# Performance work log

Measured on AMD Instinct MI355X. Metric: run time of the kernel, lower is better.

## Reference

```python
import jax, jax.numpy as jnp
import numpy as np

N = 50000
E = 800000
IN_DIM = 128
HID = 128
OUT = 4
EPS = 1e-5


def setup_inputs() -> dict:
    key = jax.random.key(0)
    ks = jax.random.split(key, 16)
    glorot = lambda k, i, o: jax.random.uniform(k, (i, o), jnp.float32, -1.0, 1.0) * jnp.sqrt(6.0 / (i + o))
    return {
        "x": jax.random.normal(ks[0], (N, IN_DIM), jnp.float32),
        "edge_index": jax.random.randint(ks[1], (2, E), 0, N, jnp.int64),
        # SAGEConv layer 0: lin_l (aggregated neighbors, with bias), lin_r (self, no bias)
        "W_l0": glorot(ks[2], IN_DIM, HID), "b_l0": jnp.zeros((HID,), jnp.float32),
        "W_r0": glorot(ks[3], IN_DIM, HID),
        # SAGEConv layer 1
        "W_l1": glorot(ks[4], HID, HID), "b_l1": jnp.zeros((HID,), jnp.float32),
        "W_r1": glorot(ks[5], HID, HID),
        # LayerNorms
        "g0": jnp.ones((HID,), jnp.float32), "beta0": jnp.zeros((HID,), jnp.float32),
        "g1": jnp.ones((HID,), jnp.float32), "beta1": jnp.zeros((HID,), jnp.float32),
        # head
        "W_h": glorot(ks[6], HID, OUT), "b_h": jnp.zeros((OUT,), jnp.float32),
    }


def _sage_conv(x, src, dst, deg_inv, W_l, b_l, W_r):
    # mean-aggregate source features at destination nodes, then project
    agg = jax.ops.segment_sum(x[src], dst, num_segments=N) * deg_inv  # [N, d]
    return agg @ W_l + b_l + x @ W_r


def _layer_norm(x, g, b):
    mu = jnp.mean(x, axis=-1, keepdims=True)
    var = jnp.mean(jnp.square(x - mu), axis=-1, keepdims=True)
    return (x - mu) * jax.lax.rsqrt(var + EPS) * g + b


def reference(x, edge_index, W_l0, b_l0, W_r0, W_l1, b_l1, W_r1, g0, beta0, g1, beta1, W_h, b_h):
    src, dst = edge_index[0], edge_index[1]
    deg = jax.ops.segment_sum(jnp.ones((E,), jnp.float32), dst, num_segments=N)
    deg_inv = (1.0 / jnp.maximum(deg, 1.0))[:, None]  # mean over empty neighborhood -> 0

    h = _sage_conv(x, src, dst, deg_inv, W_l0, b_l0, W_r0)
    h = jax.nn.relu(_layer_norm(h, g0, beta0))
    h = _sage_conv(h, src, dst, deg_inv, W_l1, b_l1, W_r1)
    h = jax.nn.relu(_layer_norm(h, g1, beta1))
    return h @ W_h + b_h  # [N, 4]
```

## Files before the change

### kernel.cpp

```cpp
#include <hip/hip_runtime.h>

#define NN 50000
#define EE 800000
#define DIM 128
#define KK 256
#define OUTD 4
#define EPSV 1e-5f
#define OTS 132
#define NB 196
#define SLOT 8192
#define ACHUNK 4096
#define NA 196

using short8v = __attribute__((ext_vector_type(8))) short;
using f32x4v  = __attribute__((ext_vector_type(4))) float;

__device__ __forceinline__ unsigned short f2bf(float f) {
    union { float f; unsigned u; } x; x.f = f;
    unsigned r = x.u + 0x7FFF + ((x.u >> 16) & 1);
    return (unsigned short)(r >> 16);
}
__device__ __forceinline__ float bf2f(unsigned short u) {
    union { unsigned u; float f; } x; x.u = ((unsigned)u) << 16;
    return x.f;
}

#define XB_BLK 6250
#define W_BLK  256
__global__ __launch_bounds__(256) void prepA_kernel(
    const float* __restrict__ x, ushort* __restrict__ xb,
    const float* __restrict__ Wl0, const float* __restrict__ Wr0,
    const float* __restrict__ Wl1, const float* __restrict__ Wr1,
    ushort* __restrict__ Wt0, ushort* __restrict__ Wt1,
    const int* __restrict__ src, const int* __restrict__ dst,
    int* __restrict__ bucketCursor, unsigned* __restrict__ pairs)
{
    int b = blockIdx.x;
    int tid = threadIdx.x;
    if (b < XB_BLK) {
        int i = b * 256 + tid;
        float4 v = ((const float4*)x)[i];
        ushort4 o;
        o.x = f2bf(v.x); o.y = f2bf(v.y); o.z = f2bf(v.z); o.w = f2bf(v.w);
        ((ushort4*)xb)[i] = o;
        return;
    }
    if (b < XB_BLK + W_BLK) {
        int idx = (b - XB_BLK) * 256 + tid;
        int which = idx >> 15;
        int j = (idx >> 8) & 127;
        int k = idx & 255;
        const float* Wl = which ? Wl1 : Wl0;
        const float* Wr = which ? Wr1 : Wr0;
        ushort* Wt = which ? Wt1 : Wt0;
        float v = (k < 128) ? Wl[k * DIM + j] : Wr[(k - 128) * DIM + j];
        Wt[j * KK + k] = f2bf(v);
        return;
    }

    __shared__ int hist[256];
    __shared__ int scanb[256];
    __shared__ int exStart[256];
    __shared__ int cur2[256];
    __shared__ int gBase[256];
    __shared__ unsigned stage[ACHUNK];
    int ab = b - XB_BLK - W_BLK;
    int eBase = ab * ACHUNK;
    int total = min(ACHUNK, EE - eBase);

    hist[tid] = 0;
    __syncthreads();

    #pragma unroll
    for (int i = 0; i < 16; i++) {
        int idx = i * 256 + tid;
        if (idx < total) {
            int d = dst[eBase + idx];
            atomicAdd(&hist[d >> 8], 1);
        }
    }
    __syncthreads();
    int cntv = hist[tid];
    scanb[tid] = cntv;
    __syncthreads();
    #pragma unroll
    for (int off = 1; off < 256; off <<= 1) {
        int add = (tid >= off) ? scanb[tid - off] : 0;
        __syncthreads();
        scanb[tid] += add;
        __syncthreads();
    }
    int ex = scanb[tid] - cntv;
    exStart[tid] = ex;
    cur2[tid] = ex;
    if (tid < NB) gBase[tid] = (cntv > 0) ? atomicAdd(&bucketCursor[tid], cntv) : 0;
    __syncthreads();

    #pragma unroll
    for (int i = 0; i < 16; i++) {
        int idx = i * 256 + tid;
        if (idx < total) {
            int e = eBase + idx;
            int d = dst[e], s = src[e];
            int bb = d >> 8;
            int sp = atomicAdd(&cur2[bb], 1);
            stage[sp] = ((unsigned)d << 16) | (unsigned)s;
        }
    }
    __syncthreads();

    #pragma unroll
    for (int i = 0; i < 16; i++) {
        int idx = i * 256 + tid;
        if (idx < total) {
            unsigned v = stage[idx];
            int bb = v >> 24;
            int pos = gBase[bb] + (idx - exStart[bb]);
            if (pos < SLOT) pairs[(size_t)bb * SLOT + pos] = v;
        }
    }
}

__global__ __launch_bounds__(256) void passB_kernel(
    const int* __restrict__ bucketCursor,
    const unsigned* __restrict__ pairs,
    int* __restrict__ rowptr, ushort* __restrict__ colS)
{
    __shared__ int bscan[256];
    __shared__ int cw[256];
    __shared__ int pre2[256];
    __shared__ unsigned val_lds[SLOT];
    int tid = threadIdx.x;
    int b = blockIdx.x;

    int c = (tid < NB) ? min(bucketCursor[tid], SLOT) : 0;
    bscan[tid] = c;
    __syncthreads();
    #pragma unroll
    for (int off = 1; off < 256; off <<= 1) {
        int add = (tid >= off) ? bscan[tid - off] : 0;
        __syncthreads();
        bscan[tid] += add;
        __syncthreads();
    }
    int myBase = b ? bscan[b - 1] : 0;
    int count  = bscan[b] - myBase;
    __syncthreads();

    cw[tid] = 0;
    __syncthreads();

    const unsigned* pb = pairs + (size_t)b * SLOT;
    for (int p = tid; p < count; p += 256) {
        unsigned v = pb[p];
        val_lds[p] = v;
        atomicAdd(&cw[(v >> 16) & 255], 1);
    }
    __syncthreads();
    int cnode = cw[tid];
    bscan[tid] = cnode;
    __syncthreads();
    #pragma unroll
    for (int off = 1; off < 256; off <<= 1) {
        int add = (tid >= off) ? bscan[tid - off] : 0;
        __syncthreads();
        bscan[tid] += add;
        __syncthreads();
    }
    int preEx = bscan[tid] - cnode;
    pre2[tid] = preEx;
    int nodeBase = b << 8;
    if (nodeBase + tid < NN) rowptr[nodeBase + tid] = myBase + preEx;
    if (b == NB - 1 && tid == 0) rowptr[NN] = myBase + count;
    cw[tid] = 0;
    __syncthreads();

    for (int p = tid; p < count; p += 256) {
        unsigned v = val_lds[p];
        int dl = (v >> 16) & 255;
        int r = atomicAdd(&cw[dl], 1);
        colS[myBase + pre2[dl] + r] = (ushort)(v & 0xFFFF);
    }
}

template <int DO_HEAD>
__global__ __launch_bounds__(256) void sage_fused_kernel(
    const ushort* __restrict__ featG,
    const int* __restrict__ rowptr, const ushort* __restrict__ colS,
    const ushort* __restrict__ WtB,
    const float* __restrict__ bl,
    const float* __restrict__ g, const float* __restrict__ beta,
    const float* __restrict__ Wh, const float* __restrict__ bh,
    void* __restrict__ outp)
{
    __shared__ __align__(16) char smem[32 * OTS * 4];
    __shared__ float mu_s[32], ri_s[32];
    ushort* featB = (ushort*)smem;
    float*  oT    = (float*)smem;
    #define OT(n, k) oT[(n) * OTS + (k)]

    int tid = threadIdx.x;
    int base = blockIdx.x * 32;
    int lane = tid & 63, w = tid >> 6;

    #pragma unroll
    for (int i = 0; i < 2; i++) {
        int idx = tid + i * 256;
        int n = idx >> 4, c = idx & 15;
        int node = base + n;
        short8v xv = {};
        if (node < NN) xv = *(const short8v*)(featG + (size_t)node * DIM + c * 8);
        int kb = (256 + c * 16) ^ ((n & 7) << 4);
        *(short8v*)(featB + n * KK + (kb >> 1)) = xv;
    }

    {
        int lane16 = lane & 15, grp = lane >> 4;
        int rp = 0;
        {
            int ridx = base + w * 8 + lane;
            if (lane < 9) rp = rowptr[min(ridx, NN)];
        }
        for (int i = 0; i < 8; i++) {
            int n = w * 8 + i;
            int beg = __shfl(rp, i, 64);
            int end = __shfl(rp, i + 1, 64);
            int deg = end - beg;
            float a0[8], a1[8];
            #pragma unroll
            for (int c = 0; c < 8; c++) { a0[c] = 0.f; a1[c] = 0.f; }
            int e = beg + grp;
            for (; e + 4 < end; e += 8) {
                int s0 = colS[e], s1 = colS[e + 4];
                short8v v0 = *(const short8v*)(featG + (size_t)s0 * DIM + lane16 * 8);
                short8v v1 = *(const short8v*)(featG + (size_t)s1 * DIM + lane16 * 8);
                #pragma unroll
                for (int c = 0; c < 8; c++) {
                    a0[c] += bf2f((unsigned short)v0[c]);
                    a1[c] += bf2f((unsigned short)v1[c]);
                }
            }
            if (e < end) {
                int s0 = colS[e];
                short8v v0 = *(const short8v*)(featG + (size_t)s0 * DIM + lane16 * 8);
                #pragma unroll
                for (int c = 0; c < 8; c++) a0[c] += bf2f((unsigned short)v0[c]);
            }
            #pragma unroll
            for (int c = 0; c < 8; c++) {
                a0[c] += a1[c];
                a0[c] += __shfl_xor(a0[c], 16, 64);
                a0[c] += __shfl_xor(a0[c], 32, 64);
            }
            if (grp == 0) {
                float di = 1.0f / fmaxf((float)deg, 1.0f);
                short8v o;
                #pragma unroll
                for (int c = 0; c < 8; c++) o[c] = (short)f2bf(a0[c] * di);
                int kb = (lane16 * 16) ^ ((n & 7) << 4);
                *(short8v*)(featB + n * KK + (kb >> 1)) = o;
            }
        }
    }
    __syncthreads();

    int l15 = lane & 15, q = lane >> 4;
    f32x4v acc00 = {}, acc01 = {}, acc10 = {}, acc11 = {};
    const ushort* wbase = WtB + (size_t)(w * 32) * KK;
    int n0 = l15, n1 = 16 + l15;
    int sw = (l15 & 7) << 4;
    #pragma unroll
    for (int ks = 0; ks < 8; ks++) {
        int kbA = ks * 64 + q * 16;
        short8v a0 = *(const short8v*)(featB + n0 * KK + (((kbA) ^ sw) >> 1));
        short8v a1 = *(const short8v*)(featB + n1 * KK + (((kbA) ^ sw) >> 1));
        int koff = ks * 32 + q * 8;
        short8v b0 = *(const short8v*)(wbase + (size_t)l15 * KK + koff);
        short8v b1 = *(const short8v*)(wbase + (size_t)(16 + l15) * KK + koff);
        acc00 = __builtin_amdgcn_mfma_f32_16x16x32_bf16(a0, b0, acc00, 0, 0, 0);
        acc01 = __builtin_amdgcn_mfma_f32_16x16x32_bf16(a0, b1, acc01, 0, 0, 0);
        acc10 = __builtin_amdgcn_mfma_f32_16x16x32_bf16(a1, b0, acc10, 0, 0, 0);
        acc11 = __builtin_amdgcn_mfma_f32_16x16x32_bf16(a1, b1, acc11, 0, 0, 0);
    }
    __syncthreads();

    {
        int c0 = w * 32 + l15, c1 = c0 + 16;
        float bl0v = bl[c0], bl1v = bl[c1];
        #pragma unroll
        for (int r = 0; r < 4; r++) {
            int r0 = q * 4 + r, r1 = 16 + q * 4 + r;
            OT(r0, c0) = acc00[r] + bl0v;
            OT(r0, c1) = acc01[r] + bl1v;
            OT(r1, c0) = acc10[r] + bl0v;
            OT(r1, c1) = acc11[r] + bl1v;
        }
    }
    __syncthreads();

    {
        int n = tid >> 3, l = tid & 7;
        float s = 0.f, s2 = 0.f;
        #pragma unroll
        for (int kk = 0; kk < 16; kk++) {
            float v = OT(n, l * 16 + kk);
            s += v; s2 += v * v;
        }
        #pragma unroll
        for (int off = 4; off; off >>= 1) {
            s  += __shfl_down(s, off, 8);
            s2 += __shfl_down(s2, off, 8);
        }
        if (l == 0) {
            float mu = s * (1.0f / DIM);
            float var = s2 * (1.0f / DIM) - mu * mu;
            mu_s[n] = mu;
            ri_s[n] = rsqrtf(fmaxf(var, 0.f) + EPSV);
        }
    }
    __syncthreads();

    if (!DO_HEAD) {
        ushort* hout = (ushort*)outp;
        #pragma unroll
        for (int i = 0; i < 16; i++) {
            int idx = tid + i * 256;
            int n = idx >> 7, k = idx & 127;
            int node = base + n;
            if (node < NN) {
                float v = (OT(n, k) - mu_s[n]) * ri_s[n] * g[k] + beta[k];
                hout[(size_t)node * DIM + k] = f2bf(fmaxf(v, 0.f));
            }
        }
    } else {
        float* fout = (float*)outp;
        float vals[16];
        #pragma unroll
        for (int i = 0; i < 16; i++) {
            int idx = tid + i * 256;
            int n = idx >> 7, k = idx & 127;
            float v = (OT(n, k) - mu_s[n]) * ri_s[n] * g[k] + beta[k];
            vals[i] = fmaxf(v, 0.f);
        }
        __syncthreads();
        #pragma unroll
        for (int i = 0; i < 16; i++) {
            int idx = tid + i * 256;
            int n = idx >> 7, k = idx & 127;
            OT(n, k) = vals[i];
        }
        __syncthreads();
        if (tid < 128) {
            int n = tid >> 2, o = tid & 3;
            int node = base + n;
            if (node < NN) {
                float s = bh[o];
                for (int k = 0; k < DIM; k++) s += OT(n, k) * Wh[k * OUTD + o];
                fout[(size_t)node * OUTD + o] = s;
            }
        }
    }
    #undef OT
}

extern "C" void kernel_launch(void* const* d_in, const int* in_sizes, int n_in,
                              void* d_out, int out_size, void* d_ws, size_t ws_size,
                              hipStream_t stream)
{
    const float* x    = (const float*)d_in[0];
    const int*   ei   = (const int*)d_in[1];
    const float* Wl0  = (const float*)d_in[2];
    const float* bl0  = (const float*)d_in[3];
    const float* Wr0  = (const float*)d_in[4];
    const float* Wl1  = (const float*)d_in[5];
    const float* bl1  = (const float*)d_in[6];
    const float* Wr1  = (const float*)d_in[7];
    const float* g0   = (const float*)d_in[8];
    const float* be0  = (const float*)d_in[9];
    const float* g1   = (const float*)d_in[10];
    const float* be1  = (const float*)d_in[11];
    const float* Wh   = (const float*)d_in[12];
    const float* bh   = (const float*)d_in[13];
    float* out = (float*)d_out;

    const int* srcI = ei;
    const int* dstI = ei + EE;

    char* p = (char*)d_ws;
    ushort*   xb     = (ushort*)p;    p += (size_t)NN * DIM * 2;
    ushort*   h      = (ushort*)p;    p += (size_t)NN * DIM * 2;
    ushort*   Wt0    = (ushort*)p;    p += DIM * KK * 2;
    ushort*   Wt1    = (ushort*)p;    p += DIM * KK * 2;
    int*      rowptr = (int*)p;       p += 50016 * 4;
    int*      bucketCursor = (int*)p; p += 256 * 4;
    unsigned* pairs  = (unsigned*)p;  p += (size_t)NB * SLOT * 4;
    ushort*   colS   = (ushort*)p;    p += (size_t)EE * 2;

    hipMemsetAsync(bucketCursor, 0, 256 * sizeof(int), stream);
    prepA_kernel<<<XB_BLK + W_BLK + NA, 256, 0, stream>>>(
        x, xb, Wl0, Wr0, Wl1, Wr1, Wt0, Wt1, srcI, dstI, bucketCursor, pairs);
    passB_kernel<<<NB, 256, 0, stream>>>(bucketCursor, pairs, rowptr, colS);

    const int blocks = (NN + 31) / 32;
    sage_fused_kernel<0><<<blocks, 256, 0, stream>>>(
        xb, rowptr, colS, Wt0, bl0, g0, be0, nullptr, nullptr, (void*)h);
    sage_fused_kernel<1><<<blocks, 256, 0, stream>>>(
        h, rowptr, colS, Wt1, bl1, g1, be1, Wh, bh, (void*)out);
}
```

Before: 214.8 us.

## Split bf16 features into column-quarter planes and gather per-thread by node

```diff
diff --git a/kernel.cpp b/kernel.cpp
--- a/kernel.cpp
+++ b/kernel.cpp
@@ -25,10 +25,11 @@
     return x.f;
 }
 
+
 #define XB_BLK 6250
 #define W_BLK  256
 __global__ __launch_bounds__(256) void prepA_kernel(
-    const float* __restrict__ x, ushort* __restrict__ xb,
+    const float* __restrict__ x, ushort* __restrict__ xqb,
     const float* __restrict__ Wl0, const float* __restrict__ Wr0,
     const float* __restrict__ Wl1, const float* __restrict__ Wr1,
     ushort* __restrict__ Wt0, ushort* __restrict__ Wt1,
@@ -42,7 +43,10 @@
         float4 v = ((const float4*)x)[i];
         ushort4 o;
         o.x = f2bf(v.x); o.y = f2bf(v.y); o.z = f2bf(v.z); o.w = f2bf(v.w);
-        ((ushort4*)xb)[i] = o;
+        int node = i >> 5;
+        int k = (i * 4) & 127;
+        int p = k >> 5, off = k & 31;
+        *(ushort4*)(xqb + ((size_t)p * NN + node) * 32 + off) = o;
         return;
     }
     if (b < XB_BLK + W_BLK) {
@@ -209,57 +213,53 @@
         int n = idx >> 4, c = idx & 15;
         int node = base + n;
         short8v xv = {};
-        if (node < NN) xv = *(const short8v*)(featG + (size_t)node * DIM + c * 8);
+        if (node < NN) {
+            int p = c >> 2;
+            int off = (c & 3) * 8;
+            xv = *(const short8v*)(featG + ((size_t)p * NN + node) * 32 + off);
+        }
         int kb = (256 + c * 16) ^ ((n & 7) << 4);
         *(short8v*)(featB + n * KK + (kb >> 1)) = xv;
     }
 
     {
-        int lane16 = lane & 15, grp = lane >> 4;
-        int rp = 0;
-        {
-            int ridx = base + w * 8 + lane;
-            if (lane < 9) rp = rowptr[min(ridx, NN)];
-        }
-        for (int i = 0; i < 8; i++) {
-            int n = w * 8 + i;
-            int beg = __shfl(rp, i, 64);
-            int end = __shfl(rp, i + 1, 64);
-            int deg = end - beg;
-            float a0[8], a1[8];
+        int n = tid >> 3;
+        int sub = tid & 7;
+        int node = base + n;
+        int beg = 0, end = 0;
+        if (node < NN) { beg = rowptr[node]; end = rowptr[node + 1]; }
+        float di = 1.0f / fmaxf((float)(end - beg), 1.0f);
+        #pragma unroll 1
+        for (int p = 0; p < 4; p++) {
+            const ushort* xq = featG + (size_t)p * NN * 32 + sub * 4;
+            float a0[4], a1[4], a2[4], a3[4];
             #pragma unroll
-            for (int c = 0; c < 8; c++) { a0[c] = 0.f; a1[c] = 0.f; }
-            int e = beg + grp;
-            for (; e + 4 < end; e += 8) {
-                int s0 = colS[e], s1 = colS[e + 4];
-                short8v v0 = *(const short8v*)(featG + (size_t)s0 * DIM + lane16 * 8);
-                short8v v1 = *(const short8v*)(featG + (size_t)s1 * DIM + lane16 * 8);
-                #pragma unroll
-                for (int c = 0; c < 8; c++) {
-                    a0[c] += bf2f((unsigned short)v0[c]);
-                    a1[c] += bf2f((unsigned short)v1[c]);
-                }
+            for (int j = 0; j < 4; j++) { a0[j] = 0.f; a1[j] = 0.f; a2[j] = 0.f; a3[j] = 0.f; }
+            int e = beg;
+            for (; e + 3 < end; e += 4) {
+                int s0 = colS[e], s1 = colS[e + 1], s2 = colS[e + 2], s3 = colS[e + 3];
+                ushort4 v0 = *(const ushort4*)(xq + s0 * 32);
+                ushort4 v1 = *(const ushort4*)(xq + s1 * 32);
+                ushort4 v2 = *(const ushort4*)(xq + s2 * 32);
+                ushort4 v3 = *(const ushort4*)(xq + s3 * 32);
+                a0[0] += bf2f(v0.x); a0[1] += bf2f(v0.y); a0[2] += bf2f(v0.z); a0[3] += bf2f(v0.w);
+                a1[0] += bf2f(v1.x); a1[1] += bf2f(v1.y); a1[2] += bf2f(v1.z); a1[3] += bf2f(v1.w);
+                a2[0] += bf2f(v2.x); a2[1] += bf2f(v2.y); a2[2] += bf2f(v2.z); a2[3] += bf2f(v2.w);
+                a3[0] += bf2f(v3.x); a3[1] += bf2f(v3.y); a3[2] += bf2f(v3.z); a3[3] += bf2f(v3.w);
             }
-            if (e < end) {
+            for (; e < end; e++) {
                 int s0 = colS[e];
-                short8v v0 = *(const short8v*)(featG + (size_t)s0 * DIM + lane16 * 8);
-                #pragma unroll
-                for (int c = 0; c < 8; c++) a0[c] += bf2f((unsigned short)v0[c]);
+                ushort4 v0 = *(const ushort4*)(xq + s0 * 32);
+                a0[0] += bf2f(v0.x); a0[1] += bf2f(v0.y); a0[2] += bf2f(v0.z); a0[3] += bf2f(v0.w);
             }
-            #pragma unroll
-            for (int c = 0; c < 8; c++) {
-                a0[c] += a1[c];
-                a0[c] += __shfl_xor(a0[c], 16, 64);
-                a0[c] += __shfl_xor(a0[c], 32, 64);
-            }
-            if (grp == 0) {
-                float di = 1.0f / fmaxf((float)deg, 1.0f);
-                short8v o;
-                #pragma unroll
-                for (int c = 0; c < 8; c++) o[c] = (short)f2bf(a0[c] * di);
-                int kb = (lane16 * 16) ^ ((n & 7) << 4);
-                *(short8v*)(featB + n * KK + (kb >> 1)) = o;
-            }
+            ushort4 o;
+            float r0 = (a0[0] + a1[0] + a2[0] + a3[0]) * di;
+            float r1 = (a0[1] + a1[1] + a2[1] + a3[1]) * di;
+            float r2 = (a0[2] + a1[2] + a2[2] + a3[2]) * di;
+            float r3 = (a0[3] + a1[3] + a2[3] + a3[3]) * di;
+            o.x = f2bf(r0); o.y = f2bf(r1); o.z = f2bf(r2); o.w = f2bf(r3);
+            int kb = (p * 64 + sub * 8) ^ ((n & 7) << 4);
+            *(ushort4*)(featB + n * KK + (kb >> 1)) = o;
         }
     }
     __syncthreads();
@@ -329,7 +329,7 @@
             int node = base + n;
             if (node < NN) {
                 float v = (OT(n, k) - mu_s[n]) * ri_s[n] * g[k] + beta[k];
-                hout[(size_t)node * DIM + k] = f2bf(fmaxf(v, 0.f));
+                hout[((size_t)(k >> 5) * NN + node) * 32 + (k & 31)] = f2bf(fmaxf(v, 0.f));
             }
         }
     } else {
@@ -387,7 +387,7 @@
     const int* dstI = ei + EE;
 
     char* p = (char*)d_ws;
-    ushort*   xb     = (ushort*)p;    p += (size_t)NN * DIM * 2;
+    ushort*   xqb    = (ushort*)p;    p += (size_t)NN * DIM * 2;
     ushort*   h      = (ushort*)p;    p += (size_t)NN * DIM * 2;
     ushort*   Wt0    = (ushort*)p;    p += DIM * KK * 2;
     ushort*   Wt1    = (ushort*)p;    p += DIM * KK * 2;
@@ -398,12 +398,12 @@
 
     hipMemsetAsync(bucketCursor, 0, 256 * sizeof(int), stream);
     prepA_kernel<<<XB_BLK + W_BLK + NA, 256, 0, stream>>>(
-        x, xb, Wl0, Wr0, Wl1, Wr1, Wt0, Wt1, srcI, dstI, bucketCursor, pairs);
+        x, xqb, Wl0, Wr0, Wl1, Wr1, Wt0, Wt1, srcI, dstI, bucketCursor, pairs);
     passB_kernel<<<NB, 256, 0, stream>>>(bucketCursor, pairs, rowptr, colS);
 
     const int blocks = (NN + 31) / 32;
     sage_fused_kernel<0><<<blocks, 256, 0, stream>>>(
-        xb, rowptr, colS, Wt0, bl0, g0, be0, nullptr, nullptr, (void*)h);
+        xqb, rowptr, colS, Wt0, bl0, g0, be0, nullptr, nullptr, (void*)h);
     sage_fused_kernel<1><<<blocks, 256, 0, stream>>>(
         h, rowptr, colS, Wt1, bl1, g1, be1, Wh, bh, (void*)out);
 }
```

After: 263.7 us. 1.23x slower.
